# Kernel tuning notes

Hardware: AMD Instinct MI355X
Metric: run time of the kernel (lower is better)

The kernel has to match this reference:

```python
import jax, jax.numpy as jnp
import numpy as np

L = 2          # n layers
P = 768        # input_p_dim
Q = 768        # input_q_dim
H = 768        # hidden (nhids[i])
A = 768        # attention dim
B, T, TQ = 16, 128, 128
EPS = 1e-6


def setup_inputs() -> dict:
    key = jax.random.key(0)
    ks = jax.random.split(key, 12)
    stdv = 1.0 / np.sqrt(H)
    u = lambda k, shp: jax.random.uniform(k, shp, jnp.float32, -stdv, stdv)
    return {
        "input_p": jax.random.normal(ks[0], (B, T, P), jnp.float32),
        "mask_p": jnp.ones((B, T), jnp.float32),
        "input_q": jax.random.normal(ks[1], (B, TQ, Q), jnp.float32),
        "mask_q": jnp.ones((B, TQ), jnp.float32),
        # LSTMCell params (stacked over layers; input size = in_d + Q = P + Q)
        "W_ih": u(ks[2], (L, P + Q, 4 * H)),
        "W_hh": u(ks[3], (L, H, 4 * H)),
        "bias": jnp.zeros((L, 4 * H), jnp.float32),
        # LayerNorm params (gamma=1, beta=0 as in reset_parameters-style init)
        "ln_i_gamma": jnp.ones((L, 4 * H), jnp.float32),
        "ln_i_beta": jnp.zeros((L, 4 * H), jnp.float32),
        "ln_h_gamma": jnp.ones((L, 4 * H), jnp.float32),
        "ln_h_beta": jnp.zeros((L, 4 * H), jnp.float32),
        "ln_c_gamma": jnp.ones((L, H), jnp.float32),
        "ln_c_beta": jnp.zeros((L, H), jnp.float32),
        # match-attention params
        "Wq": u(ks[4], (L, Q, A)),
        "Wp": u(ks[5], (L, P, A)),   # in_d == P == H for both layers
        "Wr": u(ks[6], (L, H, A)),
        "w_att": u(ks[7], (L, A)),
        "b_att": u(ks[8], (L, A)),
    }


def _layernorm(x, gamma, beta, mask):
    # Faithful to the repo's LayerNorm: mean over last dim, var over dim=1
    # (identical for 2D x), unbiased variance (torch default), eps added twice.
    mean = x.mean(-1, keepdims=True)
    var = x.var(-1, ddof=1, keepdims=True)
    out = gamma * (x - mean) / (jnp.sqrt(var + EPS) + EPS) + beta
    return out * mask[:, None]


def reference(input_p, mask_p, input_q, mask_q, W_ih, W_hh, bias,
              ln_i_gamma, ln_i_beta, ln_h_gamma, ln_h_beta,
              ln_c_gamma, ln_c_beta, Wq, Wp, Wr, w_att, b_att):
    nlayers, hid = W_hh.shape[0], W_hh.shape[1]
    bsz, tlen, _ = input_p.shape
    # q @ Wq is time-invariant: hoist out of the recurrence. (L, B, Tq, A)
    qWq = jnp.einsum("bsd,lda->lbsa", input_q, Wq)

    def step(carry, xs):
        h, c = carry                      # each (L, B, H)
        p_t, m_t = xs                     # (B, P), (B,)
        m = m_t[:, None]
        cur = p_t
        hs, cs = [], []
        for d in range(nlayers):
            # --- match attention over q, conditioned on (cur, h_tm1) ---
            s = cur @ Wp[d] + h[d] @ Wr[d] + b_att[d]          # (B, A)
            G = jnp.tanh(qWq[d] + s[:, None, :])               # (B, Tq, A)
            scores = G @ w_att[d]                              # (B, Tq)
            scores = jnp.where(mask_q > 0, scores, -1e9)
            alpha = jax.nn.softmax(scores, axis=-1)
            weighted = jnp.einsum("bs,bsd->bd", alpha, input_q)
            x = jnp.concatenate([cur, weighted], axis=-1)      # (B, in_d + Q)
            # --- LSTM cell with inline layernorm + masking ---
            wi = _layernorm(x @ W_ih[d], ln_i_gamma[d], ln_i_beta[d], m_t)
            wh = _layernorm(h[d] @ W_hh[d], ln_h_gamma[d], ln_h_beta[d], m_t)
            pre = wi + wh + bias[d]
            f, i, o, g = jnp.split(pre, 4, axis=-1)            # order: f,i,o,g
            c1 = jax.nn.sigmoid(f) * c[d] + jax.nn.sigmoid(i) * jnp.tanh(g)
            c1 = c1 * m + c[d] * (1.0 - m)
            h1 = jax.nn.sigmoid(o) * jnp.tanh(
                _layernorm(c1, ln_c_gamma[d], ln_c_beta[d], m_t))
            h1 = h1 * m + h[d] * (1.0 - m)
            hs.append(h1)
            cs.append(c1)
            cur = h1
        return (jnp.stack(hs), jnp.stack(cs)), cur             # emit top-layer h

    h0 = jnp.zeros((nlayers, bsz, hid), input_p.dtype)
    c0 = jnp.zeros_like(h0)
    xs = (jnp.transpose(input_p, (1, 0, 2)), jnp.transpose(mask_p, (1, 0)))
    _, ys = jax.lax.scan(step, (h0, c0), xs)                   # ys: (T, B, H)
    states = jnp.transpose(ys, (1, 0, 2))                      # (B, T, H)
    return (states, mask_p)
```

## Files before the change

kernel.cpp:

```cpp
#include <hip/hip_runtime.h>
#include <math.h>

#define NBLK 512
#define NTHR 256

typedef float f32x4 __attribute__((ext_vector_type(4)));

__device__ __forceinline__ float2 ld2a(const float* p){
    unsigned long long u = __hip_atomic_load((const unsigned long long*)p,
                                             __ATOMIC_RELAXED, __HIP_MEMORY_SCOPE_AGENT);
    float2 r;
    r.x = __uint_as_float((unsigned)u);
    r.y = __uint_as_float((unsigned)(u >> 32));
    return r;
}
__device__ __forceinline__ void st2a(float* p, float a, float b){
    unsigned long long u = (unsigned long long)__float_as_uint(a)
                         | ((unsigned long long)__float_as_uint(b) << 32);
    __hip_atomic_store((unsigned long long*)p, u,
                       __ATOMIC_RELAXED, __HIP_MEMORY_SCOPE_AGENT);
}
__device__ __forceinline__ float ld1a(const float* p){
    unsigned u = __hip_atomic_load((const unsigned*)p, __ATOMIC_RELAXED, __HIP_MEMORY_SCOPE_AGENT);
    return __uint_as_float(u);
}
__device__ __forceinline__ void st1a(float* p, float v){
    __hip_atomic_store((unsigned*)p, __float_as_uint(v), __ATOMIC_RELAXED, __HIP_MEMORY_SCOPE_AGENT);
}

__device__ __forceinline__ float fsigmoid(float x){ return 1.0f/(1.0f + __expf(-x)); }
__device__ __forceinline__ float ftanh(float x){
    float e = __expf(2.0f*x);
    return 1.0f - 2.0f/(e + 1.0f);
}
__device__ __forceinline__ float dot4(f32x4 a, f32x4 b){
    return a.x*b.x + a.y*b.y + a.z*b.z + a.w*b.w;
}

struct Params {
    const float* input_p; const float* mask_p; const float* input_q; const float* mask_q;
    const float* W_ih; const float* W_hh; const float* bias;
    const float* ln_i_g; const float* ln_i_b; const float* ln_h_g; const float* ln_h_b;
    const float* ln_c_g; const float* ln_c_b;
    const float* Wq; const float* Wp; const float* Wr; const float* w_att; const float* b_att;
    float* out;
    float* qWq;
    float* iqT;
    float* pWp0;
    float* pWih0;
    float* h;
    float* c;
    float* sP;
    float* whP;
    float* cwP;
    float* wiP;
    float* whR;
    float* cwR;
    float* wghtd;
    float* escore;
    unsigned* bar;
};

__device__ __forceinline__ void gsync(unsigned* bar, int bid, unsigned n){
    __syncthreads();
    if (threadIdx.x == 0){
        unsigned* leaf = bar + 128 + (bid >> 4)*32;
        unsigned old = __hip_atomic_fetch_add(leaf, 1u, __ATOMIC_RELAXED, __HIP_MEMORY_SCOPE_AGENT);
        if ((old & 15u) == 15u){
            unsigned rold = __hip_atomic_fetch_add(bar + 32, 1u, __ATOMIC_RELAXED, __HIP_MEMORY_SCOPE_AGENT);
            if ((rold & 31u) == 31u){
                __hip_atomic_store(bar, n + 1u, __ATOMIC_RELEASE, __HIP_MEMORY_SCOPE_AGENT);
            }
        }
        int spins = 0;
        while (__hip_atomic_load(bar, __ATOMIC_RELAXED, __HIP_MEMORY_SCOPE_AGENT) < n + 1u){
            __builtin_amdgcn_s_sleep(4);
            if (++spins > 1024){
                (void)__hip_atomic_load(bar, __ATOMIC_ACQUIRE, __HIP_MEMORY_SCOPE_AGENT);
                spins = 0;
            }
        }
    }
    __syncthreads();
}

__device__ __forceinline__ void stageA(
    const float* Aptr, int ars, int aco, int k0, bool coh, float* Ash, int tid)
{
    #pragma unroll
    for (int rep = 0; rep < 3; rep++){
        int i2 = tid + rep*256;
        int r = i2 / 48, kk = (i2 % 48)*2;
        const float* src = Aptr + (size_t)r*ars + aco + k0 + kk;
        float2 v;
        if (coh) v = ld2a(src); else v = *(const float2*)src;
        Ash[r*96 + kk]     = v.x;
        Ash[r*96 + kk + 1] = v.y;
    }
    __syncthreads();
}

__device__ __forceinline__ void mm96f(
    const float* W, int N, float* outP, int cbase, int k0,
    const float* Ash, int tid)
{
    int cg = tid & 15, rg = tid >> 4;
    int col = cbase + cg*8;
    f32x4 accA = {0,0,0,0}, accB = {0,0,0,0};
    const float* Wc = W + (size_t)k0*N + col;
    const float* Arow = Ash + rg*96;
    for (int kb = 0; kb < 96; kb += 4){
        f32x4 w0a = *(const f32x4*)(Wc + (size_t)(kb+0)*N);
        f32x4 w0b = *(const f32x4*)(Wc + (size_t)(kb+0)*N + 4);
        f32x4 w1a = *(const f32x4*)(Wc + (size_t)(kb+1)*N);
        f32x4 w1b = *(const f32x4*)(Wc + (size_t)(kb+1)*N + 4);
        f32x4 w2a = *(const f32x4*)(Wc + (size_t)(kb+2)*N);
        f32x4 w2b = *(const f32x4*)(Wc + (size_t)(kb+2)*N + 4);
        f32x4 w3a = *(const f32x4*)(Wc + (size_t)(kb+3)*N);
        f32x4 w3b = *(const f32x4*)(Wc + (size_t)(kb+3)*N + 4);
        float a0 = Arow[kb], a1 = Arow[kb+1], a2 = Arow[kb+2], a3 = Arow[kb+3];
        accA += a0*w0a + a1*w1a + a2*w2a + a3*w3a;
        accB += a0*w0b + a1*w1b + a2*w2b + a3*w3b;
    }
    float* o = outP + (size_t)rg*N + col;
    st2a(o,   accA.x, accA.y); st2a(o+2, accA.z, accA.w);
    st2a(o+4, accB.x, accB.y); st2a(o+6, accB.z, accB.w);
}

__device__ __forceinline__ float bsum4(float v, float* red, int tid){
    #pragma unroll
    for (int off = 32; off; off >>= 1) v += __shfl_xor(v, off);
    __syncthreads();
    if ((tid & 63) == 0) red[tid >> 6] = v;
    __syncthreads();
    float s = red[0]+red[1]+red[2]+red[3];
    __syncthreads();
    return s;
}

__global__ __launch_bounds__(NTHR, 2) void coop_kernel(Params p)
{
    __shared__ float smem[6936];
    const int tid = threadIdx.x;
    const int bid = blockIdx.x;
    unsigned n = 0;

    {
        int gid = bid*NTHR + tid;
        if (gid < 24576) st2a(p.h + gid*2, 0.f, 0.f);
        if (gid < 2048)  p.out[(size_t)16*128*768 + gid] = p.mask_p[gid];
    }
    gsync(p.bar, bid, n); n++;

    for (int t = 0; t < 128; ++t){
        for (int d = 0; d < 2; ++d){
            const float* h_d = p.h + (size_t)d*12288;

            {
                int ntile = (d == 0) ? 30 : 60;
                if (bid < ntile*8){
                    int tile = bid >> 3, kc = bid & 7, k0 = kc*96;
                    if (d == 0){
                        stageA(h_d, 768, 0, k0, true, smem, tid);
                        if (tile < 6){
                            mm96f(p.Wr, 768, p.sP + (size_t)kc*12288, tile*128, k0, smem, tid);
                        } else {
                            mm96f(p.W_hh, 3072, p.whP + (size_t)kc*49152, (tile-6)*128, k0, smem, tid);
                        }
                    } else {
                        bool useCur = (tile >= 6 && tile < 12) || (tile >= 36);
                        stageA(useCur ? p.h : h_d, 768, 0, k0, true, smem, tid);
                        if (tile < 6){
                            mm96f(p.Wr + (size_t)589824, 768,
                                  p.sP + (size_t)kc*12288, tile*128, k0, smem, tid);
                        } else if (tile < 12){
                            mm96f(p.Wp + (size_t)589824, 768,
                                  p.sP + (size_t)(8+kc)*12288, (tile-6)*128, k0, smem, tid);
                        } else if (tile < 36){
                            mm96f(p.W_hh + (size_t)2359296, 3072,
                                  p.whP + (size_t)kc*49152, (tile-12)*128, k0, smem, tid);
                        } else {
                            mm96f(p.W_ih + (size_t)4718592, 3072,
                                  p.cwP + (size_t)kc*49152, (tile-36)*128, k0, smem, tid);
                        }
                    }
                }
            }
            gsync(p.bar, bid, n); n++;

            if (bid < 256){
                int b = bid >> 4, sq0 = (bid & 15)*8;
                float* s_sh  = smem;
                float* wa_sh = smem + 768;
                if (tid < 192){
                    f32x4 acc = *(const f32x4*)(p.b_att + d*768 + tid*4);
                    if (d == 0){
                        f32x4 pv = *(const f32x4*)(p.pWp0 + ((size_t)b*128 + t)*768 + tid*4);
                        acc += pv;
                    }
                    int ncp = (d == 0) ? 8 : 16;
                    for (int cp = 0; cp < ncp; cp++){
                        const float* src = p.sP + (size_t)cp*12288 + b*768 + tid*4;
                        float2 u0 = ld2a(src);
                        float2 u1 = ld2a(src + 2);
                        acc.x += u0.x; acc.y += u0.y; acc.z += u1.x; acc.w += u1.y;
                    }
                    *(f32x4*)&s_sh[tid*4] = acc;
                } else {
                    int i0 = tid - 192;
                    for (int r = 0; r < 3; r++){
                        int i = i0 + r*64;
                        *(f32x4*)&wa_sh[i*4] = *(const f32x4*)(p.w_att + d*768 + i*4);
                    }
                }
                __syncthreads();
                int sq = sq0 + (tid >> 5), l = tid & 31;
                const float* qrow = p.qWq + ((size_t)(d*2048 + b*128 + sq))*768;
                float part = 0.f;
                #pragma unroll
                for (int i = 0; i < 6; i++){
                    int a = i*128 + l*4;
                    f32x4 q  = *(const f32x4*)(qrow + a);
                    f32x4 s4 = *(const f32x4*)(s_sh + a);
                    f32x4 w4 = *(const f32x4*)(wa_sh + a);
                    part += ftanh(q.x + s4.x)*w4.x + ftanh(q.y + s4.y)*w4.y
                          + ftanh(q.z + s4.z)*w4.z + ftanh(q.w + s4.w)*w4.w;
                }
                #pragma unroll
                for (int off = 16; off; off >>= 1) part += __shfl_xor(part, off, 32);
                if (l == 0){
                    float e = (p.mask_q[b*128 + sq] > 0.f) ? __expf(part) : 0.f;
                    st1a(p.escore + b*128 + sq, e);
                }
            }
            gsync(p.bar, bid, n); n++;

            if (bid < 64){
                int b = bid >> 2, cg = bid & 3;
                float* e_sh = smem;
                if (tid < 128) e_sh[tid] = ld1a(p.escore + b*128 + tid);
                __syncthreads();
                if (tid < 64){
                    float v = e_sh[tid] + e_sh[tid + 64];
                    #pragma unroll
                    for (int off = 32; off; off >>= 1) v += __shfl_xor(v, off);
                    if (tid == 0) e_sh[128] = 1.0f / v;
                }
                __syncthreads();
                float inv = e_sh[128];
                if (tid < 192){
                    int cc = cg*192 + tid;
                    const float* ip = p.iqT + ((size_t)b*768 + cc)*128;
                    float acc = 0.f;
                    #pragma unroll 8
                    for (int j = 0; j < 32; j++){
                        f32x4 q  = *(const f32x4*)(ip + j*4);
                        f32x4 e4 = *(const f32x4*)&e_sh[j*4];
                        acc += dot4(q, e4);
                    }
                    st1a(p.wghtd + b*768 + cc, acc*inv);
                }
            } else if (bid < 160){
                int gid = (bid - 64)*NTHR + tid;
                int which = gid / 12288;
                int i4 = gid % 12288;
                if (which == 0 || d == 1){
                    const float* src = which ? p.cwP : p.whP;
                    float* dst = which ? p.cwR : p.whR;
                    float2 a0 = {0.f,0.f}, a1 = {0.f,0.f};
                    #pragma unroll
                    for (int cp = 0; cp < 8; cp++){
                        const float* s0 = src + (size_t)cp*49152 + i4*4;
                        float2 u0 = ld2a(s0);
                        float2 u1 = ld2a(s0 + 2);
                        a0.x += u0.x; a0.y += u0.y; a1.x += u1.x; a1.y += u1.y;
                    }
                    st2a(dst + i4*4,     a0.x, a0.y);
                    st2a(dst + i4*4 + 2, a1.x, a1.y);
                }
            }
            gsync(p.bar, bid, n); n++;

            if (bid < 192){
                int tile = bid >> 3, kc = bid & 7, k0 = kc*96;
                stageA(p.wghtd, 768, 0, k0, true, smem, tid);
                mm96f(p.W_ih + (size_t)d*4718592 + (size_t)768*3072, 3072,
                      p.wiP + (size_t)kc*49152, tile*128, k0, smem, tid);
            }
            gsync(p.bar, bid, n); n++;

            if (bid < 16){
                const int b = bid;
                float* wi_sh = smem;
                float* wh_sh = smem + 3072;
                float* c_sh  = smem + 6144;
                float* red   = smem + 6928;
                const float mm = p.mask_p[b*128 + t];
                const float* gi = p.ln_i_g + d*3072; const float* bi = p.ln_i_b + d*3072;
                const float* gh = p.ln_h_g + d*3072; const float* bh = p.ln_h_b + d*3072;
                const float* gc = p.ln_c_g + d*768;  const float* bc = p.ln_c_b + d*768;
                const float* bias_d = p.bias + d*3072;

                float swi=0,qwi=0,swh=0,qwh=0;
                #pragma unroll
                for (int rep = 0; rep < 3; rep++){
                    int j4 = tid + rep*256;
                    int base = b*3072 + j4*4;
                    f32x4 a = {0,0,0,0};
                    #pragma unroll
                    for (int cp = 0; cp < 8; cp++){
                        const float* s0 = p.wiP + (size_t)cp*49152 + base;
                        float2 u0 = ld2a(s0);
                        float2 u1 = ld2a(s0 + 2);
                        a.x += u0.x; a.y += u0.y; a.z += u1.x; a.w += u1.y;
                    }
                    if (d == 0){
                        f32x4 pv = *(const f32x4*)(p.pWih0 + ((size_t)b*128 + t)*3072 + j4*4);
                        a += pv;
                    } else {
                        float2 cw0 = ld2a(p.cwR + base), cw1 = ld2a(p.cwR + base + 2);
                        a.x += cw0.x; a.y += cw0.y; a.z += cw1.x; a.w += cw1.y;
                    }
                    float2 wh0 = ld2a(p.whR + base), wh1 = ld2a(p.whR + base + 2);
                    f32x4 hvec = { wh0.x, wh0.y, wh1.x, wh1.y };
                    *(f32x4*)&wi_sh[j4*4] = a;
                    *(f32x4*)&wh_sh[j4*4] = hvec;
                    swi += a.x+a.y+a.z+a.w;
                    qwi += dot4(a,a);
                    swh += hvec.x+hvec.y+hvec.z+hvec.w;
                    qwh += dot4(hvec,hvec);
                }
                swi = bsum4(swi, red, tid);
                qwi = bsum4(qwi, red, tid);
                swh = bsum4(swh, red, tid);
                qwh = bsum4(qwh, red, tid);
                float mi = swi/3072.f, vi = fmaxf((qwi - 3072.f*mi*mi)/3071.f, 0.f);
                float mh = swh/3072.f, vh = fmaxf((qwh - 3072.f*mh*mh)/3071.f, 0.f);
                float ivi = 1.f/(sqrtf(vi + 1e-6f) + 1e-6f);
                float ivh = 1.f/(sqrtf(vh + 1e-6f) + 1e-6f);

                for (int j = tid; j < 3072; j += NTHR){
                    float pre = mm*(gi[j]*(wi_sh[j]-mi)*ivi + bi[j])
                              + mm*(gh[j]*(wh_sh[j]-mh)*ivh + bh[j])
                              + bias_d[j];
                    wi_sh[j] = pre;
                }
                __syncthreads();

                float sc=0,qc=0;
                for (int idx = tid; idx < 384; idx += NTHR){
                    int u = idx*2;
                    float2 c_old = ld2a(p.c + (size_t)d*12288 + b*768 + u);
                    float f0  = wi_sh[u],        f1  = wi_sh[u+1];
                    float i0  = wi_sh[768+u],    i1  = wi_sh[768+u+1];
                    float g0  = wi_sh[2304+u],   g1  = wi_sh[2304+u+1];
                    float c10 = fsigmoid(f0)*c_old.x + fsigmoid(i0)*ftanh(g0);
                    float c11 = fsigmoid(f1)*c_old.y + fsigmoid(i1)*ftanh(g1);
                    c10 = c10*mm + c_old.x*(1.f - mm);
                    c11 = c11*mm + c_old.y*(1.f - mm);
                    st2a(p.c + (size_t)d*12288 + b*768 + u, c10, c11);
                    c_sh[u] = c10; c_sh[u+1] = c11;
                    sc += c10 + c11; qc += c10*c10 + c11*c11;
                }
                sc = bsum4(sc, red, tid);
                qc = bsum4(qc, red, tid);
                float mc = sc/768.f, vc = fmaxf((qc - 768.f*mc*mc)/767.f, 0.f);
                float ivc = 1.f/(sqrtf(vc + 1e-6f) + 1e-6f);

                for (int idx = tid; idx < 384; idx += NTHR){
                    int u = idx*2;
                    float2 h_old = ld2a(p.h + (size_t)d*12288 + b*768 + u);
                    float o0 = wi_sh[1536+u], o1 = wi_sh[1536+u+1];
                    float l0 = (gc[u]*(c_sh[u]-mc)*ivc + bc[u])*mm;
                    float l1 = (gc[u+1]*(c_sh[u+1]-mc)*ivc + bc[u+1])*mm;
                    float h10 = fsigmoid(o0)*ftanh(l0);
                    float h11 = fsigmoid(o1)*ftanh(l1);
                    h10 = h10*mm + h_old.x*(1.f - mm);
                    h11 = h11*mm + h_old.y*(1.f - mm);
                    st2a(p.h + (size_t)d*12288 + b*768 + u, h10, h11);
                    if (d == 1){
                        float2 ov = { h10, h11 };
                        *(float2*)(p.out + ((size_t)b*128 + t)*768 + u) = ov;
                    }
                }
            }
            gsync(p.bar, bid, n); n++;
        }
    }
}

__global__ __launch_bounds__(256) void k_mm_pre(
    const float* __restrict__ Ain, const float* __restrict__ W,
    float* __restrict__ C, int ldw, int ncols)
{
    __shared__ float Ash[16][772];
    int rowbase = blockIdx.y*16;
    for (int r = 0; r < 16; r++)
        for (int i = threadIdx.x; i < 768; i += 256)
            Ash[r][i] = Ain[(size_t)(rowbase + r)*768 + i];
    __syncthreads();
    int lane = threadIdx.x & 63;
    int colq = lane & 15, rsub = lane >> 4, wq = threadIdx.x >> 6;
    int r = wq*4 + rsub;
    int col = blockIdx.x*64 + colq*4;
    float4 acc = {0.f,0.f,0.f,0.f};
    const float* Wc = W + col;
    for (int k = 0; k < 768; k += 4){
        float4 a4 = *(const float4*)&Ash[r][k];
        float4 w0 = *(const float4*)(Wc + (size_t)(k+0)*ldw);
        float4 w1 = *(const float4*)(Wc + (size_t)(k+1)*ldw);
        float4 w2 = *(const float4*)(Wc + (size_t)(k+2)*ldw);
        float4 w3 = *(const float4*)(Wc + (size_t)(k+3)*ldw);
        acc.x += a4.x*w0.x + a4.y*w1.x + a4.z*w2.x + a4.w*w3.x;
        acc.y += a4.x*w0.y + a4.y*w1.y + a4.z*w2.y + a4.w*w3.y;
        acc.z += a4.x*w0.z + a4.y*w1.z + a4.z*w2.z + a4.w*w3.z;
        acc.w += a4.x*w0.w + a4.y*w1.w + a4.z*w2.w + a4.w*w3.w;
    }
    *(float4*)(C + (size_t)(rowbase + r)*ncols + col) = acc;
}

__global__ __launch_bounds__(256) void k_transq(
    const float* __restrict__ iq, float* __restrict__ iqT)
{
    __shared__ float Tsh[32][136];
    int c0 = blockIdx.x*32, b = blockIdx.y;
    for (int rep = 0; rep < 4; rep++){
        int idx = threadIdx.x + rep*256;
        int sq = idx >> 3, cq = idx & 7;
        float4 v = *(const float4*)(iq + ((size_t)b*128 + sq)*768 + c0 + cq*4);
        Tsh[cq*4+0][sq] = v.x;
        Tsh[cq*4+1][sq] = v.y;
        Tsh[cq*4+2][sq] = v.z;
        Tsh[cq*4+3][sq] = v.w;
    }
    __syncthreads();
    for (int rep = 0; rep < 4; rep++){
        int idx = threadIdx.x + rep*256;
        int cl = idx >> 5, sq4 = (idx & 31)*4;
        float4 v = *(const float4*)&Tsh[cl][sq4];
        *(float4*)(iqT + ((size_t)b*768 + c0 + cl)*128 + sq4) = v;
    }
}

extern "C" void kernel_launch(void* const* d_in, const int* in_sizes, int n_in,
                              void* d_out, int out_size, void* d_ws, size_t ws_size,
                              hipStream_t stream)
{
    (void)in_sizes; (void)n_in; (void)out_size; (void)ws_size;
    Params P;
    P.input_p = (const float*)d_in[0];
    P.mask_p  = (const float*)d_in[1];
    P.input_q = (const float*)d_in[2];
    P.mask_q  = (const float*)d_in[3];
    P.W_ih    = (const float*)d_in[4];
    P.W_hh    = (const float*)d_in[5];
    P.bias    = (const float*)d_in[6];
    P.ln_i_g  = (const float*)d_in[7];
    P.ln_i_b  = (const float*)d_in[8];
    P.ln_h_g  = (const float*)d_in[9];
    P.ln_h_b  = (const float*)d_in[10];
    P.ln_c_g  = (const float*)d_in[11];
    P.ln_c_b  = (const float*)d_in[12];
    P.Wq      = (const float*)d_in[13];
    P.Wp      = (const float*)d_in[14];
    P.Wr      = (const float*)d_in[15];
    P.w_att   = (const float*)d_in[16];
    P.b_att   = (const float*)d_in[17];
    P.out     = (float*)d_out;

    float* ws = (float*)d_ws;
    size_t off = 0;
    auto alloc = [&](size_t nfloat)->float*{
        float* r = ws + off;
        off += (nfloat + 63) & ~(size_t)63;
        return r;
    };
    P.qWq    = alloc((size_t)2*2048*768);
    P.iqT    = alloc((size_t)16*768*128);
    P.pWp0   = alloc((size_t)2048*768);
    P.pWih0  = alloc((size_t)2048*3072);
    P.h      = alloc(24576);
    P.c      = alloc(24576);
    P.sP     = alloc((size_t)16*16*768);
    P.whP    = alloc((size_t)8*16*3072);
    P.cwP    = alloc((size_t)8*16*3072);
    P.wiP    = alloc((size_t)8*16*3072);
    P.whR    = alloc(49152);
    P.cwR    = alloc(49152);
    P.wghtd  = alloc(12288);
    P.escore = alloc(2048);
    P.bar    = (unsigned*)alloc(2048);

    hipMemsetAsync((void*)P.bar, 0, 2048*sizeof(unsigned), stream);
    k_mm_pre<<<dim3(12,128), 256, 0, stream>>>(P.input_q, P.Wq, P.qWq, 768, 768);
    k_mm_pre<<<dim3(12,128), 256, 0, stream>>>(P.input_q, P.Wq + (size_t)589824,
                                               P.qWq + (size_t)2048*768, 768, 768);
    k_mm_pre<<<dim3(12,128), 256, 0, stream>>>(P.input_p, P.Wp, P.pWp0, 768, 768);
    k_mm_pre<<<dim3(48,128), 256, 0, stream>>>(P.input_p, P.W_ih, P.pWih0, 3072, 3072);
    k_transq<<<dim3(24,16), 256, 0, stream>>>(P.input_q, P.iqT);
    coop_kernel<<<dim3(NBLK), dim3(NTHR), 0, stream>>>(P);
}
```

Baseline: 17.59 ms.

## Halve split-K factor, narrow column tiles, fold partial reductions into consumers

The recurrent matvec tiles now split K into 4 chunks of 192 and use 64-column tiles instead of 8 chunks of 96 with 128 columns. Each thread handles 4 columns with a double-buffered register prefetch of weight rows. The separate partial-sum reduction pass for whP/cwP (whR/cwR) is removed, and the LSTM stage sums the 4 partials directly. This halves the partial-buffer traffic and drops the extra reduction work. The trade-off is that the LSTM blocks do more coherent loads.

```diff
diff --git a/kernel.cpp b/kernel.cpp
--- a/kernel.cpp
+++ b/kernel.cpp
@@ -54,8 +54,6 @@
     float* whP;
     float* cwP;
     float* wiP;
-    float* whR;
-    float* cwR;
     float* wghtd;
     float* escore;
     unsigned* bar;
@@ -88,43 +86,45 @@
     const float* Aptr, int ars, int aco, int k0, bool coh, float* Ash, int tid)
 {
     #pragma unroll
-    for (int rep = 0; rep < 3; rep++){
+    for (int rep = 0; rep < 6; rep++){
         int i2 = tid + rep*256;
-        int r = i2 / 48, kk = (i2 % 48)*2;
+        int r = i2 / 96, kk = (i2 % 96)*2;
         const float* src = Aptr + (size_t)r*ars + aco + k0 + kk;
         float2 v;
         if (coh) v = ld2a(src); else v = *(const float2*)src;
-        Ash[r*96 + kk]     = v.x;
-        Ash[r*96 + kk + 1] = v.y;
-    }
-    __syncthreads();
-}
-
-__device__ __forceinline__ void mm96f(
+        Ash[r*192 + kk]     = v.x;
+        Ash[r*192 + kk + 1] = v.y;
+    }
+    __syncthreads();
+}
+
+__device__ __forceinline__ void mm192f(
     const float* W, int N, float* outP, int cbase, int k0,
     const float* Ash, int tid)
 {
     int cg = tid & 15, rg = tid >> 4;
-    int col = cbase + cg*8;
-    f32x4 accA = {0,0,0,0}, accB = {0,0,0,0};
+    int col = cbase + cg*4;
     const float* Wc = W + (size_t)k0*N + col;
-    const float* Arow = Ash + rg*96;
-    for (int kb = 0; kb < 96; kb += 4){
-        f32x4 w0a = *(const f32x4*)(Wc + (size_t)(kb+0)*N);
-        f32x4 w0b = *(const f32x4*)(Wc + (size_t)(kb+0)*N + 4);
-        f32x4 w1a = *(const f32x4*)(Wc + (size_t)(kb+1)*N);
-        f32x4 w1b = *(const f32x4*)(Wc + (size_t)(kb+1)*N + 4);
-        f32x4 w2a = *(const f32x4*)(Wc + (size_t)(kb+2)*N);
-        f32x4 w2b = *(const f32x4*)(Wc + (size_t)(kb+2)*N + 4);
-        f32x4 w3a = *(const f32x4*)(Wc + (size_t)(kb+3)*N);
-        f32x4 w3b = *(const f32x4*)(Wc + (size_t)(kb+3)*N + 4);
-        float a0 = Arow[kb], a1 = Arow[kb+1], a2 = Arow[kb+2], a3 = Arow[kb+3];
-        accA += a0*w0a + a1*w1a + a2*w2a + a3*w3a;
-        accB += a0*w0b + a1*w1b + a2*w2b + a3*w3b;
+    const float* Arow = Ash + rg*192;
+    f32x4 acc = {0,0,0,0};
+    f32x4 wA[8], wB[8];
+    #pragma unroll
+    for (int j = 0; j < 8; j++) wA[j] = *(const f32x4*)(Wc + (size_t)j*N);
+    for (int kb = 0; kb < 192; kb += 16){
+        #pragma unroll
+        for (int j = 0; j < 8; j++) wB[j] = *(const f32x4*)(Wc + (size_t)(kb+8+j)*N);
+        #pragma unroll
+        for (int j = 0; j < 8; j++) acc += Arow[kb+j]*wA[j];
+        if (kb < 176){
+            #pragma unroll
+            for (int j = 0; j < 8; j++) wA[j] = *(const f32x4*)(Wc + (size_t)(kb+16+j)*N);
+        }
+        #pragma unroll
+        for (int j = 0; j < 8; j++) acc += Arow[kb+8+j]*wB[j];
     }
     float* o = outP + (size_t)rg*N + col;
-    st2a(o,   accA.x, accA.y); st2a(o+2, accA.z, accA.w);
-    st2a(o+4, accB.x, accB.y); st2a(o+6, accB.z, accB.w);
+    st2a(o,   acc.x, acc.y);
+    st2a(o+2, acc.z, acc.w);
 }
 
 __device__ __forceinline__ float bsum4(float v, float* red, int tid){
@@ -157,31 +157,31 @@
             const float* h_d = p.h + (size_t)d*12288;
 
             {
-                int ntile = (d == 0) ? 30 : 60;
-                if (bid < ntile*8){
-                    int tile = bid >> 3, kc = bid & 7, k0 = kc*96;
+                int ntile = (d == 0) ? 60 : 120;
+                if (bid < ntile*4){
+                    int tile = bid >> 2, kc = bid & 3, k0 = kc*192;
                     if (d == 0){
                         stageA(h_d, 768, 0, k0, true, smem, tid);
-                        if (tile < 6){
-                            mm96f(p.Wr, 768, p.sP + (size_t)kc*12288, tile*128, k0, smem, tid);
+                        if (tile < 12){
+                            mm192f(p.Wr, 768, p.sP + (size_t)kc*12288, tile*64, k0, smem, tid);
                         } else {
-                            mm96f(p.W_hh, 3072, p.whP + (size_t)kc*49152, (tile-6)*128, k0, smem, tid);
+                            mm192f(p.W_hh, 3072, p.whP + (size_t)kc*49152, (tile-12)*64, k0, smem, tid);
                         }
                     } else {
-                        bool useCur = (tile >= 6 && tile < 12) || (tile >= 36);
+                        bool useCur = (tile >= 12 && tile < 24) || (tile >= 72);
                         stageA(useCur ? p.h : h_d, 768, 0, k0, true, smem, tid);
-                        if (tile < 6){
-                            mm96f(p.Wr + (size_t)589824, 768,
-                                  p.sP + (size_t)kc*12288, tile*128, k0, smem, tid);
-                        } else if (tile < 12){
-                            mm96f(p.Wp + (size_t)589824, 768,
-                                  p.sP + (size_t)(8+kc)*12288, (tile-6)*128, k0, smem, tid);
-                        } else if (tile < 36){
-                            mm96f(p.W_hh + (size_t)2359296, 3072,
-                                  p.whP + (size_t)kc*49152, (tile-12)*128, k0, smem, tid);
+                        if (tile < 12){
+                            mm192f(p.Wr + (size_t)589824, 768,
+                                   p.sP + (size_t)kc*12288, tile*64, k0, smem, tid);
+                        } else if (tile < 24){
+                            mm192f(p.Wp + (size_t)589824, 768,
+                                   p.sP + (size_t)(4+kc)*12288, (tile-12)*64, k0, smem, tid);
+                        } else if (tile < 72){
+                            mm192f(p.W_hh + (size_t)2359296, 3072,
+                                   p.whP + (size_t)kc*49152, (tile-24)*64, k0, smem, tid);
                         } else {
-                            mm96f(p.W_ih + (size_t)4718592, 3072,
-                                  p.cwP + (size_t)kc*49152, (tile-36)*128, k0, smem, tid);
+                            mm192f(p.W_ih + (size_t)4718592, 3072,
+                                   p.cwP + (size_t)kc*49152, (tile-72)*64, k0, smem, tid);
                         }
                     }
                 }
@@ -198,7 +198,7 @@
                         f32x4 pv = *(const f32x4*)(p.pWp0 + ((size_t)b*128 + t)*768 + tid*4);
                         acc += pv;
                     }
-                    int ncp = (d == 0) ? 8 : 16;
+                    int ncp = (d == 0) ? 4 : 8;
                     for (int cp = 0; cp < ncp; cp++){
                         const float* src = p.sP + (size_t)cp*12288 + b*768 + tid*4;
                         float2 u0 = ld2a(src);
@@ -260,32 +260,14 @@
                     }
                     st1a(p.wghtd + b*768 + cc, acc*inv);
                 }
-            } else if (bid < 160){
-                int gid = (bid - 64)*NTHR + tid;
-                int which = gid / 12288;
-                int i4 = gid % 12288;
-                if (which == 0 || d == 1){
-                    const float* src = which ? p.cwP : p.whP;
-                    float* dst = which ? p.cwR : p.whR;
-                    float2 a0 = {0.f,0.f}, a1 = {0.f,0.f};
-                    #pragma unroll
-                    for (int cp = 0; cp < 8; cp++){
-                        const float* s0 = src + (size_t)cp*49152 + i4*4;
-                        float2 u0 = ld2a(s0);
-                        float2 u1 = ld2a(s0 + 2);
-                        a0.x += u0.x; a0.y += u0.y; a1.x += u1.x; a1.y += u1.y;
-                    }
-                    st2a(dst + i4*4,     a0.x, a0.y);
-                    st2a(dst + i4*4 + 2, a1.x, a1.y);
-                }
             }
             gsync(p.bar, bid, n); n++;
 
             if (bid < 192){
-                int tile = bid >> 3, kc = bid & 7, k0 = kc*96;
+                int tile = bid >> 2, kc = bid & 3, k0 = kc*192;
                 stageA(p.wghtd, 768, 0, k0, true, smem, tid);
-                mm96f(p.W_ih + (size_t)d*4718592 + (size_t)768*3072, 3072,
-                      p.wiP + (size_t)kc*49152, tile*128, k0, smem, tid);
+                mm192f(p.W_ih + (size_t)d*4718592 + (size_t)768*3072, 3072,
+                       p.wiP + (size_t)kc*49152, tile*64, k0, smem, tid);
             }
             gsync(p.bar, bid, n); n++;
 
@@ -307,22 +289,30 @@
                     int j4 = tid + rep*256;
                     int base = b*3072 + j4*4;
                     f32x4 a = {0,0,0,0};
+                    f32x4 hvec = {0,0,0,0};
                     #pragma unroll
-                    for (int cp = 0; cp < 8; cp++){
+                    for (int cp = 0; cp < 4; cp++){
                         const float* s0 = p.wiP + (size_t)cp*49152 + base;
                         float2 u0 = ld2a(s0);
                         float2 u1 = ld2a(s0 + 2);
                         a.x += u0.x; a.y += u0.y; a.z += u1.x; a.w += u1.y;
+                        const float* s1 = p.whP + (size_t)cp*49152 + base;
+                        float2 v0 = ld2a(s1);
+                        float2 v1 = ld2a(s1 + 2);
+                        hvec.x += v0.x; hvec.y += v0.y; hvec.z += v1.x; hvec.w += v1.y;
                     }
                     if (d == 0){
                         f32x4 pv = *(const f32x4*)(p.pWih0 + ((size_t)b*128 + t)*3072 + j4*4);
                         a += pv;
                     } else {
-                        float2 cw0 = ld2a(p.cwR + base), cw1 = ld2a(p.cwR + base + 2);
-                        a.x += cw0.x; a.y += cw0.y; a.z += cw1.x; a.w += cw1.y;
-                    }
-                    float2 wh0 = ld2a(p.whR + base), wh1 = ld2a(p.whR + base + 2);
-                    f32x4 hvec = { wh0.x, wh0.y, wh1.x, wh1.y };
+                        #pragma unroll
+                        for (int cp = 0; cp < 4; cp++){
+                            const float* s2 = p.cwP + (size_t)cp*49152 + base;
+                            float2 w0 = ld2a(s2);
+                            float2 w1 = ld2a(s2 + 2);
+                            a.x += w0.x; a.y += w0.y; a.z += w1.x; a.w += w1.y;
+                        }
+                    }
                     *(f32x4*)&wi_sh[j4*4] = a;
                     *(f32x4*)&wh_sh[j4*4] = hvec;
                     swi += a.x+a.y+a.z+a.w;
@@ -481,12 +471,10 @@
     P.pWih0  = alloc((size_t)2048*3072);
     P.h      = alloc(24576);
     P.c      = alloc(24576);
-    P.sP     = alloc((size_t)16*16*768);
-    P.whP    = alloc((size_t)8*16*3072);
-    P.cwP    = alloc((size_t)8*16*3072);
-    P.wiP    = alloc((size_t)8*16*3072);
-    P.whR    = alloc(49152);
-    P.cwR    = alloc(49152);
+    P.sP     = alloc((size_t)8*16*768);
+    P.whP    = alloc((size_t)4*16*3072);
+    P.cwP    = alloc((size_t)4*16*3072);
+    P.wiP    = alloc((size_t)4*16*3072);
     P.wghtd  = alloc(12288);
     P.escore = alloc(2048);
     P.bar    = (unsigned*)alloc(2048);
```

Measured after the change: 18.70 ms. +6.3%, slower.

## Scale persistent kernel to 768 blocks with finer K-split GEMM phases

Applied to the files above, without the earlier changes.

Raises the persistent cooperative kernel from 512 to 768 blocks at three blocks per CU, and adjusts the tree barrier to the new count. The recurrent GEMMs are split into 12 K-chunks of 64 instead of 8 of 96, with the partial-sum reductions updated to match. The attention-score phase is spread over 512 blocks, and the weighted-input GEMM moves to 64-column tiles with a K-split of 4 chunks of 192. The aim is to use more CUs and shorten each serial phase of the recurrence, at the cost of more partial buffers to reduce, a larger barrier, and register pressure from the tighter launch bound.

```diff
diff --git a/kernel.cpp b/kernel.cpp
--- a/kernel.cpp
+++ b/kernel.cpp
@@ -1,7 +1,7 @@
 #include <hip/hip_runtime.h>
 #include <math.h>
 
-#define NBLK 512
+#define NBLK 768
 #define NTHR 256
 
 typedef float f32x4 __attribute__((ext_vector_type(4)));
@@ -68,7 +68,7 @@
         unsigned old = __hip_atomic_fetch_add(leaf, 1u, __ATOMIC_RELAXED, __HIP_MEMORY_SCOPE_AGENT);
         if ((old & 15u) == 15u){
             unsigned rold = __hip_atomic_fetch_add(bar + 32, 1u, __ATOMIC_RELAXED, __HIP_MEMORY_SCOPE_AGENT);
-            if ((rold & 31u) == 31u){
+            if ((rold % 48u) == 47u){
                 __hip_atomic_store(bar, n + 1u, __ATOMIC_RELEASE, __HIP_MEMORY_SCOPE_AGENT);
             }
         }
@@ -84,47 +84,80 @@
     __syncthreads();
 }
 
-__device__ __forceinline__ void stageA(
-    const float* Aptr, int ars, int aco, int k0, bool coh, float* Ash, int tid)
-{
+__device__ __forceinline__ void stageA64(const float* src, int k0, float* Ash, int tid){
     #pragma unroll
-    for (int rep = 0; rep < 3; rep++){
+    for (int rep = 0; rep < 2; rep++){
         int i2 = tid + rep*256;
-        int r = i2 / 48, kk = (i2 % 48)*2;
-        const float* src = Aptr + (size_t)r*ars + aco + k0 + kk;
-        float2 v;
-        if (coh) v = ld2a(src); else v = *(const float2*)src;
-        Ash[r*96 + kk]     = v.x;
-        Ash[r*96 + kk + 1] = v.y;
-    }
-    __syncthreads();
-}
-
-__device__ __forceinline__ void mm96f(
+        int r = i2 >> 5, kk = (i2 & 31)*2;
+        float2 v = ld2a(src + (size_t)r*768 + k0 + kk);
+        Ash[r*68 + kk]     = v.x;
+        Ash[r*68 + kk + 1] = v.y;
+    }
+    __syncthreads();
+}
+
+__device__ __forceinline__ void stageA192(const float* src, int k0, float* Ash, int tid){
+    #pragma unroll
+    for (int rep = 0; rep < 6; rep++){
+        int i2 = tid + rep*256;
+        int r = i2 / 96, kk = (i2 % 96)*2;
+        float2 v = ld2a(src + (size_t)r*768 + k0 + kk);
+        Ash[r*196 + kk]     = v.x;
+        Ash[r*196 + kk + 1] = v.y;
+    }
+    __syncthreads();
+}
+
+__device__ __forceinline__ void mm64(
     const float* W, int N, float* outP, int cbase, int k0,
     const float* Ash, int tid)
 {
     int cg = tid & 15, rg = tid >> 4;
     int col = cbase + cg*8;
-    f32x4 accA = {0,0,0,0}, accB = {0,0,0,0};
     const float* Wc = W + (size_t)k0*N + col;
-    const float* Arow = Ash + rg*96;
-    for (int kb = 0; kb < 96; kb += 4){
-        f32x4 w0a = *(const f32x4*)(Wc + (size_t)(kb+0)*N);
-        f32x4 w0b = *(const f32x4*)(Wc + (size_t)(kb+0)*N + 4);
-        f32x4 w1a = *(const f32x4*)(Wc + (size_t)(kb+1)*N);
-        f32x4 w1b = *(const f32x4*)(Wc + (size_t)(kb+1)*N + 4);
-        f32x4 w2a = *(const f32x4*)(Wc + (size_t)(kb+2)*N);
-        f32x4 w2b = *(const f32x4*)(Wc + (size_t)(kb+2)*N + 4);
-        f32x4 w3a = *(const f32x4*)(Wc + (size_t)(kb+3)*N);
-        f32x4 w3b = *(const f32x4*)(Wc + (size_t)(kb+3)*N + 4);
-        float a0 = Arow[kb], a1 = Arow[kb+1], a2 = Arow[kb+2], a3 = Arow[kb+3];
-        accA += a0*w0a + a1*w1a + a2*w2a + a3*w3a;
-        accB += a0*w0b + a1*w1b + a2*w2b + a3*w3b;
+    const float* Arow = Ash + rg*68;
+    f32x4 acc0 = {0,0,0,0}, acc1 = {0,0,0,0};
+    for (int kb = 0; kb < 64; kb += 8){
+        f32x4 wa[8], wb[8];
+        #pragma unroll
+        for (int j = 0; j < 8; j++){
+            wa[j] = *(const f32x4*)(Wc + (size_t)(kb+j)*N);
+            wb[j] = *(const f32x4*)(Wc + (size_t)(kb+j)*N + 4);
+        }
+        #pragma unroll
+        for (int j = 0; j < 8; j++){
+            float a = Arow[kb + j];
+            acc0 += a*wa[j];
+            acc1 += a*wb[j];
+        }
     }
     float* o = outP + (size_t)rg*N + col;
-    st2a(o,   accA.x, accA.y); st2a(o+2, accA.z, accA.w);
-    st2a(o+4, accB.x, accB.y); st2a(o+6, accB.z, accB.w);
+    st2a(o,   acc0.x, acc0.y); st2a(o+2, acc0.z, acc0.w);
+    st2a(o+4, acc1.x, acc1.y); st2a(o+6, acc1.z, acc1.w);
+    __syncthreads();
+}
+
+__device__ __forceinline__ void mm192(
+    const float* W, int N, float* outP, int cbase, int k0,
+    const float* Ash, int tid)
+{
+    int cg = tid & 15, rg = tid >> 4;
+    int col = cbase + cg*4;
+    const float* Wc = W + (size_t)k0*N + col;
+    const float* Arow = Ash + rg*196;
+    f32x4 acc = {0,0,0,0};
+    for (int kb = 0; kb < 192; kb += 8){
+        f32x4 w[8];
+        #pragma unroll
+        for (int j = 0; j < 8; j++)
+            w[j] = *(const f32x4*)(Wc + (size_t)(kb+j)*N);
+        #pragma unroll
+        for (int j = 0; j < 8; j++)
+            acc += Arow[kb + j]*w[j];
+    }
+    float* o = outP + (size_t)rg*N + col;
+    st2a(o,   acc.x, acc.y); st2a(o+2, acc.z, acc.w);
+    __syncthreads();
 }
 
 __device__ __forceinline__ float bsum4(float v, float* red, int tid){
@@ -138,7 +171,7 @@
     return s;
 }
 
-__global__ __launch_bounds__(NTHR, 2) void coop_kernel(Params p)
+__global__ __launch_bounds__(NTHR, 3) void coop_kernel(Params p)
 {
     __shared__ float smem[6936];
     const int tid = threadIdx.x;
@@ -147,58 +180,53 @@
 
     {
         int gid = bid*NTHR + tid;
-        if (gid < 24576) st2a(p.h + gid*2, 0.f, 0.f);
+        if (gid < 24576) st2a(p.h + (size_t)gid*2, 0.f, 0.f);
         if (gid < 2048)  p.out[(size_t)16*128*768 + gid] = p.mask_p[gid];
     }
     gsync(p.bar, bid, n); n++;
 
     for (int t = 0; t < 128; ++t){
         for (int d = 0; d < 2; ++d){
-            const float* h_d = p.h + (size_t)d*12288;
 
             {
-                int ntile = (d == 0) ? 30 : 60;
-                if (bid < ntile*8){
-                    int tile = bid >> 3, kc = bid & 7, k0 = kc*96;
+                int nblk = (d == 0) ? 360 : 720;
+                if (bid < nblk){
+                    int tile = bid / 12, kc = bid % 12, k0 = kc*64;
                     if (d == 0){
-                        stageA(h_d, 768, 0, k0, true, smem, tid);
-                        if (tile < 6){
-                            mm96f(p.Wr, 768, p.sP + (size_t)kc*12288, tile*128, k0, smem, tid);
-                        } else {
-                            mm96f(p.W_hh, 3072, p.whP + (size_t)kc*49152, (tile-6)*128, k0, smem, tid);
-                        }
+                        stageA64(p.h, k0, smem, tid);
+                        if (tile < 6)
+                            mm64(p.Wr, 768, p.sP + (size_t)kc*12288, tile*128, k0, smem, tid);
+                        else
+                            mm64(p.W_hh, 3072, p.whP + (size_t)kc*49152, (tile-6)*128, k0, smem, tid);
                     } else {
-                        bool useCur = (tile >= 6 && tile < 12) || (tile >= 36);
-                        stageA(useCur ? p.h : h_d, 768, 0, k0, true, smem, tid);
-                        if (tile < 6){
-                            mm96f(p.Wr + (size_t)589824, 768,
-                                  p.sP + (size_t)kc*12288, tile*128, k0, smem, tid);
-                        } else if (tile < 12){
-                            mm96f(p.Wp + (size_t)589824, 768,
-                                  p.sP + (size_t)(8+kc)*12288, (tile-6)*128, k0, smem, tid);
-                        } else if (tile < 36){
-                            mm96f(p.W_hh + (size_t)2359296, 3072,
-                                  p.whP + (size_t)kc*49152, (tile-12)*128, k0, smem, tid);
-                        } else {
-                            mm96f(p.W_ih + (size_t)4718592, 3072,
-                                  p.cwP + (size_t)kc*49152, (tile-36)*128, k0, smem, tid);
-                        }
+                        bool useH1 = (tile < 6) || (tile >= 12 && tile < 36);
+                        stageA64(p.h + (useH1 ? 12288 : 0), k0, smem, tid);
+                        if (tile < 6)
+                            mm64(p.Wr + (size_t)589824, 768,
+                                 p.sP + (size_t)kc*12288, tile*128, k0, smem, tid);
+                        else if (tile < 12)
+                            mm64(p.Wp + (size_t)589824, 768,
+                                 p.sP + (size_t)(12+kc)*12288, (tile-6)*128, k0, smem, tid);
+                        else if (tile < 36)
+                            mm64(p.W_hh + (size_t)2359296, 3072,
+                                 p.whP + (size_t)kc*49152, (tile-12)*128, k0, smem, tid);
+                        else
+                            mm64(p.W_ih + (size_t)4718592, 3072,
+                                 p.cwP + (size_t)kc*49152, (tile-36)*128, k0, smem, tid);
                     }
                 }
             }
             gsync(p.bar, bid, n); n++;
 
-            if (bid < 256){
-                int b = bid >> 4, sq0 = (bid & 15)*8;
+            if (bid < 512){
+                int b = bid >> 5, sq0 = (bid & 31)*4;
                 float* s_sh  = smem;
                 float* wa_sh = smem + 768;
                 if (tid < 192){
                     f32x4 acc = *(const f32x4*)(p.b_att + d*768 + tid*4);
-                    if (d == 0){
-                        f32x4 pv = *(const f32x4*)(p.pWp0 + ((size_t)b*128 + t)*768 + tid*4);
-                        acc += pv;
-                    }
-                    int ncp = (d == 0) ? 8 : 16;
+                    if (d == 0)
+                        acc += *(const f32x4*)(p.pWp0 + ((size_t)b*128 + t)*768 + tid*4);
+                    int ncp = (d == 0) ? 12 : 24;
                     for (int cp = 0; cp < ncp; cp++){
                         const float* src = p.sP + (size_t)cp*12288 + b*768 + tid*4;
                         float2 u0 = ld2a(src);
@@ -208,26 +236,27 @@
                     *(f32x4*)&s_sh[tid*4] = acc;
                 } else {
                     int i0 = tid - 192;
-                    for (int r = 0; r < 3; r++){
-                        int i = i0 + r*64;
+                    for (int rr = 0; rr < 3; rr++){
+                        int i = i0 + rr*64;
                         *(f32x4*)&wa_sh[i*4] = *(const f32x4*)(p.w_att + d*768 + i*4);
                     }
                 }
                 __syncthreads();
-                int sq = sq0 + (tid >> 5), l = tid & 31;
-                const float* qrow = p.qWq + ((size_t)(d*2048 + b*128 + sq))*768;
+                int sq = sq0 + (tid >> 6), l = tid & 63;
+                const float* qrow = p.qWq + ((size_t)(d*2048 + b*128 + sq))*768 + l*12;
+                const float* ss = s_sh + l*12;
+                const float* ww = wa_sh + l*12;
                 float part = 0.f;
                 #pragma unroll
-                for (int i = 0; i < 6; i++){
-                    int a = i*128 + l*4;
-                    f32x4 q  = *(const f32x4*)(qrow + a);
-                    f32x4 s4 = *(const f32x4*)(s_sh + a);
-                    f32x4 w4 = *(const f32x4*)(wa_sh + a);
+                for (int i = 0; i < 3; i++){
+                    f32x4 q  = *(const f32x4*)(qrow + i*4);
+                    f32x4 s4 = *(const f32x4*)(ss + i*4);
+                    f32x4 w4 = *(const f32x4*)(ww + i*4);
                     part += ftanh(q.x + s4.x)*w4.x + ftanh(q.y + s4.y)*w4.y
                           + ftanh(q.z + s4.z)*w4.z + ftanh(q.w + s4.w)*w4.w;
                 }
                 #pragma unroll
-                for (int off = 16; off; off >>= 1) part += __shfl_xor(part, off, 32);
+                for (int off = 32; off; off >>= 1) part += __shfl_xor(part, off);
                 if (l == 0){
                     float e = (p.mask_q[b*128 + sq] > 0.f) ? __expf(part) : 0.f;
                     st1a(p.escore + b*128 + sq, e);
@@ -262,14 +291,15 @@
                 }
             } else if (bid < 160){
                 int gid = (bid - 64)*NTHR + tid;
-                int which = gid / 12288;
-                int i4 = gid % 12288;
-                if (which == 0 || d == 1){
+                int ntask = d ? 24576 : 12288;
+                if (gid < ntask){
+                    int which = gid >= 12288;
+                    int i4 = which ? gid - 12288 : gid;
                     const float* src = which ? p.cwP : p.whP;
                     float* dst = which ? p.cwR : p.whR;
                     float2 a0 = {0.f,0.f}, a1 = {0.f,0.f};
                     #pragma unroll
-                    for (int cp = 0; cp < 8; cp++){
+                    for (int cp = 0; cp < 12; cp++){
                         const float* s0 = src + (size_t)cp*49152 + i4*4;
                         float2 u0 = ld2a(s0);
                         float2 u1 = ld2a(s0 + 2);
@@ -282,10 +312,10 @@
             gsync(p.bar, bid, n); n++;
 
             if (bid < 192){
-                int tile = bid >> 3, kc = bid & 7, k0 = kc*96;
-                stageA(p.wghtd, 768, 0, k0, true, smem, tid);
-                mm96f(p.W_ih + (size_t)d*4718592 + (size_t)768*3072, 3072,
-                      p.wiP + (size_t)kc*49152, tile*128, k0, smem, tid);
+                int tile = bid >> 2, kc = bid & 3, k0 = kc*192;
+                stageA192(p.wghtd, k0, smem, tid);
+                mm192(p.W_ih + (size_t)d*4718592 + (size_t)2359296, 3072,
+                      p.wiP + (size_t)kc*49152, tile*64, k0, smem, tid);
             }
             gsync(p.bar, bid, n); n++;
 
@@ -295,7 +325,7 @@
                 float* wh_sh = smem + 3072;
                 float* c_sh  = smem + 6144;
                 float* red   = smem + 6928;
-                const float mm = p.mask_p[b*128 + t];
+                const float mmv = p.mask_p[b*128 + t];
                 const float* gi = p.ln_i_g + d*3072; const float* bi = p.ln_i_b + d*3072;
                 const float* gh = p.ln_h_g + d*3072; const float* bh = p.ln_h_b + d*3072;
                 const float* gc = p.ln_c_g + d*768;  const float* bc = p.ln_c_b + d*768;
@@ -308,27 +338,24 @@
                     int base = b*3072 + j4*4;
                     f32x4 a = {0,0,0,0};
                     #pragma unroll
-                    for (int cp = 0; cp < 8; cp++){
+                    for (int cp = 0; cp < 4; cp++){
                         const float* s0 = p.wiP + (size_t)cp*49152 + base;
                         float2 u0 = ld2a(s0);
                         float2 u1 = ld2a(s0 + 2);
                         a.x += u0.x; a.y += u0.y; a.z += u1.x; a.w += u1.y;
                     }
                     if (d == 0){
-                        f32x4 pv = *(const f32x4*)(p.pWih0 + ((size_t)b*128 + t)*3072 + j4*4);
-                        a += pv;
+                        a += *(const f32x4*)(p.pWih0 + ((size_t)b*128 + t)*3072 + j4*4);
                     } else {
-                        float2 cw0 = ld2a(p.cwR + base), cw1 = ld2a(p.cwR + base + 2);
-                        a.x += cw0.x; a.y += cw0.y; a.z += cw1.x; a.w += cw1.y;
-                    }
-                    float2 wh0 = ld2a(p.whR + base), wh1 = ld2a(p.whR + base + 2);
-                    f32x4 hvec = { wh0.x, wh0.y, wh1.x, wh1.y };
+                        float2 c0 = ld2a(p.cwR + base), c1 = ld2a(p.cwR + base + 2);
+                        a.x += c0.x; a.y += c0.y; a.z += c1.x; a.w += c1.y;
+                    }
+                    float2 h0 = ld2a(p.whR + base), h1 = ld2a(p.whR + base + 2);
+                    f32x4 hvec = { h0.x, h0.y, h1.x, h1.y };
                     *(f32x4*)&wi_sh[j4*4] = a;
                     *(f32x4*)&wh_sh[j4*4] = hvec;
-                    swi += a.x+a.y+a.z+a.w;
-                    qwi += dot4(a,a);
-                    swh += hvec.x+hvec.y+hvec.z+hvec.w;
-                    qwh += dot4(hvec,hvec);
+                    swi += a.x+a.y+a.z+a.w;   qwi += dot4(a,a);
+                    swh += hvec.x+hvec.y+hvec.z+hvec.w; qwh += dot4(hvec,hvec);
                 }
                 swi = bsum4(swi, red, tid);
                 qwi = bsum4(qwi, red, tid);
@@ -340,8 +367,8 @@
                 float ivh = 1.f/(sqrtf(vh + 1e-6f) + 1e-6f);
 
                 for (int j = tid; j < 3072; j += NTHR){
-                    float pre = mm*(gi[j]*(wi_sh[j]-mi)*ivi + bi[j])
-                              + mm*(gh[j]*(wh_sh[j]-mh)*ivh + bh[j])
+                    float pre = mmv*(gi[j]*(wi_sh[j]-mi)*ivi + bi[j])
+                              + mmv*(gh[j]*(wh_sh[j]-mh)*ivh + bh[j])
                               + bias_d[j];
                     wi_sh[j] = pre;
                 }
@@ -356,8 +383,8 @@
                     float g0  = wi_sh[2304+u],   g1  = wi_sh[2304+u+1];
                     float c10 = fsigmoid(f0)*c_old.x + fsigmoid(i0)*ftanh(g0);
                     float c11 = fsigmoid(f1)*c_old.y + fsigmoid(i1)*ftanh(g1);
-                    c10 = c10*mm + c_old.x*(1.f - mm);
-                    c11 = c11*mm + c_old.y*(1.f - mm);
+                    c10 = c10*mmv + c_old.x*(1.f - mmv);
+                    c11 = c11*mmv + c_old.y*(1.f - mmv);
                     st2a(p.c + (size_t)d*12288 + b*768 + u, c10, c11);
                     c_sh[u] = c10; c_sh[u+1] = c11;
                     sc += c10 + c11; qc += c10*c10 + c11*c11;
@@ -371,18 +398,19 @@
                     int u = idx*2;
                     float2 h_old = ld2a(p.h + (size_t)d*12288 + b*768 + u);
                     float o0 = wi_sh[1536+u], o1 = wi_sh[1536+u+1];
-                    float l0 = (gc[u]*(c_sh[u]-mc)*ivc + bc[u])*mm;
-                    float l1 = (gc[u+1]*(c_sh[u+1]-mc)*ivc + bc[u+1])*mm;
+                    float l0 = (gc[u]*(c_sh[u]-mc)*ivc + bc[u])*mmv;
+                    float l1 = (gc[u+1]*(c_sh[u+1]-mc)*ivc + bc[u+1])*mmv;
                     float h10 = fsigmoid(o0)*ftanh(l0);
                     float h11 = fsigmoid(o1)*ftanh(l1);
-                    h10 = h10*mm + h_old.x*(1.f - mm);
-                    h11 = h11*mm + h_old.y*(1.f - mm);
+                    h10 = h10*mmv + h_old.x*(1.f - mmv);
+                    h11 = h11*mmv + h_old.y*(1.f - mmv);
                     st2a(p.h + (size_t)d*12288 + b*768 + u, h10, h11);
                     if (d == 1){
                         float2 ov = { h10, h11 };
                         *(float2*)(p.out + ((size_t)b*128 + t)*768 + u) = ov;
                     }
                 }
+                __syncthreads();
             }
             gsync(p.bar, bid, n); n++;
         }
@@ -481,10 +509,10 @@
     P.pWih0  = alloc((size_t)2048*3072);
     P.h      = alloc(24576);
     P.c      = alloc(24576);
-    P.sP     = alloc((size_t)16*16*768);
-    P.whP    = alloc((size_t)8*16*3072);
-    P.cwP    = alloc((size_t)8*16*3072);
-    P.wiP    = alloc((size_t)8*16*3072);
+    P.sP     = alloc((size_t)24*12288);
+    P.whP    = alloc((size_t)12*49152);
+    P.cwP    = alloc((size_t)12*49152);
+    P.wiP    = alloc((size_t)4*49152);
     P.whR    = alloc(49152);
     P.cwR    = alloc(49152);
     P.wghtd  = alloc(12288);
```

After: 28.17 ms. 60.1% more time.
